# Performance work log

Measured on AMD Instinct MI355X. Metric: run time of the kernel, lower is better.

Reference implementation:

```python
import jax, jax.numpy as jnp
import numpy as np

N_WIN = 8      # windows per side (j = i = n_win)
NUM_HEADS = 8
TOPK = 4


def setup_inputs() -> dict:
    key = jax.random.key(0)
    k1, k2 = jax.random.split(key)
    cv_feature = jax.random.normal(k1, (1, 128, 128, 256), dtype=jnp.float32)
    mv_feature = jax.random.normal(k2, (1, 4, 128, 128, 256), dtype=jnp.float32)
    return {"cv_feature": cv_feature, "mv_feature": mv_feature}


def reference(cv_feature, mv_feature):
    n, H, W, C = cv_feature.shape
    v = mv_feature.shape[1]
    j = i = N_WIN
    h, w = H // j, W // i
    p2, w2 = j * i, h * w
    m = NUM_HEADS
    ch = C // m
    scale = C ** (-0.5)  # module uses d_model**-0.5 for both routing and pixel attn

    # window partition: n (j h)(i w) c -> n (j i) h w c
    cv_patch = cv_feature.reshape(n, j, h, i, w, C).transpose(0, 1, 3, 2, 4, 5).reshape(n, p2, h, w, C)
    mv_patch = mv_feature.reshape(n, v, j, h, i, w, C).transpose(0, 1, 2, 4, 3, 5, 6).reshape(n, v, p2, h, w, C)

    q_pix = cv_patch.reshape(n, p2, w2, C)          # n p2 w2 c
    kv_pix = mv_patch.reshape(n, v, p2, w2, C)      # n v p2 w2 c

    # window-level pooled queries/keys (routing is detached in the original)
    q_win = jax.lax.stop_gradient(cv_patch.mean((2, 3)))            # n p2 c
    k_win = jax.lax.stop_gradient(mv_patch.mean((3, 4)))            # n v p2 c
    k_win = k_win.reshape(n, v * p2, C)

    logits = jnp.einsum('npc,nqc->npq', q_win * scale, k_win)       # n p2 (v p2)
    topk_logit, r_idx = jax.lax.top_k(logits, TOPK)                 # n p2 k
    r_weight = jax.nn.softmax(topk_logit, axis=-1)                  # computed, unused (faithful)

    # gather routed KV windows: n p2 k w2 c
    kv_flat = kv_pix.reshape(n, v * p2, w2, C)
    kv_sel = jnp.take_along_axis(kv_flat[:, None], r_idx[:, :, :, None, None], axis=2)

    # split heads
    k_sel = kv_sel.reshape(n, p2, TOPK, w2, m, ch)                  # n p2 k w2 m ch
    q = q_pix.reshape(n, p2, w2, m, ch)                             # n p2 w2 m ch

    attn = jnp.einsum('npqmc,npkwmc->npmqkw', q * scale, k_sel)
    attn = attn.reshape(n, p2, m, w2, TOPK * w2)
    attn = jax.nn.softmax(attn, axis=-1)

    v_sel = k_sel.transpose(0, 1, 4, 2, 3, 5).reshape(n, p2, m, TOPK * w2, ch)
    out = jnp.einsum('npmqt,npmtc->npmqc', attn, v_sel)             # n p2 m w2 ch

    # merge heads + window un-partition: -> n H W C
    out = out.transpose(0, 1, 3, 2, 4).reshape(n, j, i, h, w, C)
    out = out.transpose(0, 1, 3, 2, 4, 5).reshape(n, H, W, C)
    return out
```

## Files before the change

kernel.cpp:

```cpp
#include <hip/hip_runtime.h>
#include <hip/hip_bf16.h>


typedef __attribute__((ext_vector_type(4))) float f32x4;
typedef __attribute__((ext_vector_type(8))) short s16x8;
typedef __attribute__((ext_vector_type(4))) short s16x4;
typedef __attribute__((ext_vector_type(2))) unsigned u32x2;
typedef __attribute__((ext_vector_type(4))) unsigned u32x4;

#define SCALE 0.0625f
#define LOG2E 1.44269504088896340736f

__device__ inline unsigned cvt_pk_bf16(float lo, float hi) {
  unsigned r;
  asm("v_cvt_pk_bf16_f32 %0, %1, %2" : "=v"(r) : "v"(lo), "v"(hi));
  return r;
}
__device__ inline unsigned pk_bf16_rne(float lo, float hi) {
  unsigned a = __float_as_uint(lo);
  unsigned b = __float_as_uint(hi);
  a += 0x7FFFu + ((a >> 16) & 1u);
  b += 0x7FFFu + ((b >> 16) & 1u);
  return (a >> 16) | (b & 0xFFFF0000u);
}
#if __has_builtin(__builtin_amdgcn_exp2f)
#define EXP2(x) __builtin_amdgcn_exp2f(x)
#else
#define EXP2(x) exp2f(x)
#endif

__global__ __launch_bounds__(256) void k_means(const float* __restrict__ cv,
                                               const float* __restrict__ mv,
                                               float* __restrict__ qwin,
                                               float* __restrict__ kwin) {
  __shared__ float sm[4][64];
  int wi = blockIdx.x >> 2, cq = blockIdx.x & 3;
  int pq = threadIdx.x >> 6, cl = threadIdx.x & 63;
  int c = cq * 64 + cl;
  const float* base;
  float* dst;
  if (wi < 64) {
    base = cv + ((size_t)((wi >> 3) * 16) * 128 + (wi & 7) * 16) * 256;
    dst = qwin + wi * 256;
  } else {
    int r = wi - 64;
    base = mv + (size_t)(r >> 6) * (128 * 128 * 256)
         + ((size_t)(((r >> 3) & 7) * 16) * 128 + (r & 7) * 16) * 256;
    dst = kwin + r * 256;
  }
  float s = 0.f;
  for (int k = 0; k < 64; ++k) {
    int px = pq * 64 + k;
    s += base[((px >> 4) * 128 + (px & 15)) * 256 + c];
  }
  sm[pq][cl] = s;
  __syncthreads();
  if (pq == 0)
    dst[c] = (sm[0][cl] + sm[1][cl] + sm[2][cl] + sm[3][cl]) * (1.f / 256.f);
}

__global__ __launch_bounds__(256) void k_route(const float* __restrict__ qwin,
                                               const float* __restrict__ kwin,
                                               int* __restrict__ ridx) {
  __shared__ float qrow[256];
  __shared__ float sv[256];
  __shared__ float wbv[4];
  __shared__ int wbi[4];
  int p = blockIdx.x, t = threadIdx.x;
  qrow[t] = qwin[p * 256 + t] * SCALE;
  __syncthreads();
  const f32x4* kr = reinterpret_cast<const f32x4*>(kwin + t * 256);
  float dot = 0.f;
#pragma unroll 4
  for (int c4 = 0; c4 < 64; ++c4) {
    f32x4 kv = kr[c4];
    dot += qrow[c4 * 4 + 0] * kv[0] + qrow[c4 * 4 + 1] * kv[1]
         + qrow[c4 * 4 + 2] * kv[2] + qrow[c4 * 4 + 3] * kv[3];
  }
  sv[t] = dot;
  __syncthreads();
  for (int k = 0; k < 4; ++k) {
    float v = sv[t];
    int ii = t;
#pragma unroll
    for (int off = 32; off > 0; off >>= 1) {
      float ov = __shfl_down(v, off, 64);
      int oi = __shfl_down(ii, off, 64);
      if (ov > v || (ov == v && oi < ii)) { v = ov; ii = oi; }
    }
    if ((t & 63) == 0) { wbv[t >> 6] = v; wbi[t >> 6] = ii; }
    __syncthreads();
    if (t == 0) {
      float bv = wbv[0]; int bi = wbi[0];
      for (int j = 1; j < 4; ++j)
        if (wbv[j] > bv || (wbv[j] == bv && wbi[j] < bi)) { bv = wbv[j]; bi = wbi[j]; }
      ridx[p * 4 + k] = bi;
      sv[bi] = -3.0e38f;
    }
    __syncthreads();
  }
}

__global__ __launch_bounds__(256, 2) void k_attn(const float* __restrict__ cv,
                                                 const float* __restrict__ mv,
                                                 const int* __restrict__ ridx,
                                                 float* __restrict__ out) {
  __shared__ __align__(16) short kv_lds[256 * 32];

  const int tid = threadIdx.x;
  const int lane = tid & 63, wv = tid >> 6;
  const int g = lane >> 4, c16 = lane & 15;
  const int p = blockIdx.x >> 3, m = blockIdx.x & 7;
  const int py = p >> 3, px = p & 7;

  const int4 ridx4 = *reinterpret_cast<const int4*>(ridx + p * 4);

  const float qs = SCALE * LOG2E;
  s16x8 qf[4];
#pragma unroll
  for (int qt = 0; qt < 4; ++qt) {
    const float* qp = cv + ((size_t)((py * 16 + wv * 4 + qt) * 128) + px * 16 + c16) * 256
                         + m * 32 + g * 8;
    f32x4 a = *reinterpret_cast<const f32x4*>(qp);
    f32x4 b = *reinterpret_cast<const f32x4*>(qp + 4);
    union { u32x4 u; s16x8 s; } cu;
    cu.u[0] = cvt_pk_bf16(a[0] * qs, a[1] * qs);
    cu.u[1] = cvt_pk_bf16(a[2] * qs, a[3] * qs);
    cu.u[2] = cvt_pk_bf16(b[0] * qs, b[1] * qs);
    cu.u[3] = cvt_pk_bf16(b[2] * qs, b[3] * qs);
    qf[qt] = cu.s;
  }

  f32x4 accO[4][2];
  float lsum[4];
#pragma unroll
  for (int qt = 0; qt < 4; ++qt) {
    lsum[qt] = 0.f;
    accO[qt][0] = f32x4{0.f, 0.f, 0.f, 0.f};
    accO[qt][1] = f32x4{0.f, 0.f, 0.f, 0.f};
  }
  const f32x4 zf = {0.f, 0.f, 0.f, 0.f};

  for (int w = 0; w < 4; ++w) {
    if (w) __syncthreads();
    {
      int r = (&ridx4.x)[w];
      const float* srcb = mv + (size_t)(r >> 6) * (128 * 128 * 256)
                        + ((size_t)(((r >> 3) & 7) * 16) * 128 + (r & 7) * 16) * 256 + m * 32;
#pragma unroll
      for (int i = 0; i < 8; ++i) {
        int u = i * 256 + tid;
        int pxl = u >> 3, quad = u & 7;
        f32x4 d = *reinterpret_cast<const f32x4*>(
            srcb + ((pxl >> 4) * 128 + (pxl & 15)) * 256 + quad * 4);
        u32x2 pk;
        pk[0] = cvt_pk_bf16(d[0], d[1]);
        pk[1] = cvt_pk_bf16(d[2], d[3]);
        int off = (pxl >> 2) * 128 + (quad >> 2) * 64 + (pxl & 3) * 16 + (quad & 3) * 4;
        *reinterpret_cast<u32x2*>(&kv_lds[off]) = pk;
      }
    }
    __syncthreads();

    for (int s = 0; s < 8; ++s) {
      int kr0 = s * 32 + c16;
      int kr1 = kr0 + 16;
      const s16x8 kf0 = *reinterpret_cast<const s16x8*>(
          &kv_lds[(kr0 >> 2) * 128 + (g >> 1) * 64 + (kr0 & 3) * 16 + (g & 1) * 8]);
      const s16x8 kf1 = *reinterpret_cast<const s16x8*>(
          &kv_lds[(kr1 >> 2) * 128 + (g >> 1) * 64 + (kr1 & 3) * 16 + (g & 1) * 8]);
      s16x8 V0, V1;
#pragma unroll
      for (int j = 0; j < 8; ++j) {
        int a = (s * 8 + (j >> 2) * 4 + g) * 128 + (j & 3) * 16 + c16;
        V0[j] = kv_lds[a];
        V1[j] = kv_lds[a + 64];
      }
#pragma unroll
      for (int qt = 0; qt < 4; ++qt) {
        f32x4 sx = __builtin_amdgcn_mfma_f32_16x16x32_bf16(kf0, qf[qt], zf, 0, 0, 0);
        f32x4 sy = __builtin_amdgcn_mfma_f32_16x16x32_bf16(kf1, qf[qt], zf, 0, 0, 0);
        float x0 = EXP2(sx[0]), x1 = EXP2(sx[1]), x2 = EXP2(sx[2]), x3 = EXP2(sx[3]);
        float y0 = EXP2(sy[0]), y1 = EXP2(sy[1]), y2 = EXP2(sy[2]), y3 = EXP2(sy[3]);
        lsum[qt] += ((x0 + x1) + (x2 + x3)) + ((y0 + y1) + (y2 + y3));
        union { u32x4 u; s16x8 s; } pb;
        pb.u[0] = pk_bf16_rne(x0, x1);
        pb.u[1] = pk_bf16_rne(x2, x3);
        pb.u[2] = pk_bf16_rne(y0, y1);
        pb.u[3] = pk_bf16_rne(y2, y3);
        accO[qt][0] = __builtin_amdgcn_mfma_f32_16x16x32_bf16(V0, pb.s, accO[qt][0], 0, 0, 0);
        accO[qt][1] = __builtin_amdgcn_mfma_f32_16x16x32_bf16(V1, pb.s, accO[qt][1], 0, 0, 0);
      }
    }
  }

#pragma unroll
  for (int qt = 0; qt < 4; ++qt) {
    float l = lsum[qt];
    l += __shfl_xor(l, 16, 64);
    l += __shfl_xor(l, 32, 64);
    float rl = 1.f / l;
#pragma unroll
    for (int mt = 0; mt < 2; ++mt) {
      f32x4 o = accO[qt][mt];
      o[0] *= rl; o[1] *= rl; o[2] *= rl; o[3] *= rl;
      float* op = out + ((size_t)((py * 16 + wv * 4 + qt) * 128) + px * 16 + c16) * 256
                      + m * 32 + mt * 16 + g * 4;
      *reinterpret_cast<f32x4*>(op) = o;
    }
  }
}

extern "C" void kernel_launch(void* const* d_in, const int* in_sizes, int n_in,
                              void* d_out, int out_size, void* d_ws, size_t ws_size,
                              hipStream_t stream) {
  const float* cv = (const float*)d_in[0];
  const float* mv = (const float*)d_in[1];
  float* out = (float*)d_out;

  float* qwin = (float*)d_ws;
  float* kwin = qwin + 64 * 256;
  int* ridx = (int*)(kwin + 256 * 256);

  k_means<<<1280, 256, 0, stream>>>(cv, mv, qwin, kwin);
  k_route<<<64, 256, 0, stream>>>(qwin, kwin, ridx);
  k_attn<<<512, 256, 0, stream>>>(cv, mv, ridx, out);
}
```

Before: 71.77 us.

## Vectorize window means, compute softmax denominator via MFMA, cheaper bf16 packing

The window-mean kernel now has each thread load float4 and handle half the channels per block, so it launches half as many blocks and issues fewer, wider loads. In the attention kernel the row-sum of exponentials moves from VALU adds plus cross-lane shuffles to an extra MFMA against a ones matrix. The same row sum is then available in every output lane. Probability packing to bf16 switches from round-to-nearest-even to a round-half-away add plus a byte permute, which takes fewer instructions. The trade-offs are one extra MFMA per tile and a slightly different rounding mode for the probabilities.

```diff
diff --git a/kernel.cpp b/kernel.cpp
--- a/kernel.cpp
+++ b/kernel.cpp
@@ -4,7 +4,6 @@
 
 typedef __attribute__((ext_vector_type(4))) float f32x4;
 typedef __attribute__((ext_vector_type(8))) short s16x8;
-typedef __attribute__((ext_vector_type(4))) short s16x4;
 typedef __attribute__((ext_vector_type(2))) unsigned u32x2;
 typedef __attribute__((ext_vector_type(4))) unsigned u32x4;
 
@@ -16,12 +15,10 @@
   asm("v_cvt_pk_bf16_f32 %0, %1, %2" : "=v"(r) : "v"(lo), "v"(hi));
   return r;
 }
-__device__ inline unsigned pk_bf16_rne(float lo, float hi) {
-  unsigned a = __float_as_uint(lo);
-  unsigned b = __float_as_uint(hi);
-  a += 0x7FFFu + ((a >> 16) & 1u);
-  b += 0x7FFFu + ((b >> 16) & 1u);
-  return (a >> 16) | (b & 0xFFFF0000u);
+__device__ inline unsigned pk_bf16_rna(float lo, float hi) {
+  unsigned a = __float_as_uint(lo) + 0x8000u;
+  unsigned b = __float_as_uint(hi) + 0x8000u;
+  return __builtin_amdgcn_perm(b, a, 0x07060302u);
 }
 #if __has_builtin(__builtin_amdgcn_exp2f)
 #define EXP2(x) __builtin_amdgcn_exp2f(x)
@@ -33,10 +30,9 @@
                                                const float* __restrict__ mv,
                                                float* __restrict__ qwin,
                                                float* __restrict__ kwin) {
-  __shared__ float sm[4][64];
-  int wi = blockIdx.x >> 2, cq = blockIdx.x & 3;
-  int pq = threadIdx.x >> 6, cl = threadIdx.x & 63;
-  int c = cq * 64 + cl;
+  __shared__ f32x4 sm[8][32];
+  int wi = blockIdx.x >> 1, half = blockIdx.x & 1;
+  int c4 = threadIdx.x & 31, pq = threadIdx.x >> 5;
   const float* base;
   float* dst;
   if (wi < 64) {
@@ -48,15 +44,23 @@
          + ((size_t)(((r >> 3) & 7) * 16) * 128 + (r & 7) * 16) * 256;
     dst = kwin + r * 256;
   }
-  float s = 0.f;
-  for (int k = 0; k < 64; ++k) {
-    int px = pq * 64 + k;
-    s += base[((px >> 4) * 128 + (px & 15)) * 256 + c];
-  }
-  sm[pq][cl] = s;
+  base += half * 128 + c4 * 4;
+  f32x4 acc = {0.f, 0.f, 0.f, 0.f};
+#pragma unroll 4
+  for (int k = 0; k < 32; ++k) {
+    int px = pq * 32 + k;
+    f32x4 d = *reinterpret_cast<const f32x4*>(base + ((px >> 4) * 128 + (px & 15)) * 256);
+    acc += d;
+  }
+  sm[pq][c4] = acc;
   __syncthreads();
-  if (pq == 0)
-    dst[c] = (sm[0][cl] + sm[1][cl] + sm[2][cl] + sm[3][cl]) * (1.f / 256.f);
+  if (pq == 0) {
+    f32x4 s = sm[0][c4];
+#pragma unroll
+    for (int j = 1; j < 8; ++j) s += sm[j][c4];
+    s *= (1.f / 256.f);
+    *reinterpret_cast<f32x4*>(dst + half * 128 + c4 * 4) = s;
+  }
 }
 
 __global__ __launch_bounds__(256) void k_route(const float* __restrict__ qwin,
@@ -131,11 +135,15 @@
     qf[qt] = cu.s;
   }
 
+  union { u32x4 u; s16x8 s; } ones;
+#pragma unroll
+  for (int j = 0; j < 4; ++j) ones.u[j] = 0x3F803F80u;
+
   f32x4 accO[4][2];
-  float lsum[4];
+  f32x4 accL[4];
 #pragma unroll
   for (int qt = 0; qt < 4; ++qt) {
-    lsum[qt] = 0.f;
+    accL[qt] = f32x4{0.f, 0.f, 0.f, 0.f};
     accO[qt][0] = f32x4{0.f, 0.f, 0.f, 0.f};
     accO[qt][1] = f32x4{0.f, 0.f, 0.f, 0.f};
   }
@@ -182,24 +190,21 @@
         f32x4 sy = __builtin_amdgcn_mfma_f32_16x16x32_bf16(kf1, qf[qt], zf, 0, 0, 0);
         float x0 = EXP2(sx[0]), x1 = EXP2(sx[1]), x2 = EXP2(sx[2]), x3 = EXP2(sx[3]);
         float y0 = EXP2(sy[0]), y1 = EXP2(sy[1]), y2 = EXP2(sy[2]), y3 = EXP2(sy[3]);
-        lsum[qt] += ((x0 + x1) + (x2 + x3)) + ((y0 + y1) + (y2 + y3));
         union { u32x4 u; s16x8 s; } pb;
-        pb.u[0] = pk_bf16_rne(x0, x1);
-        pb.u[1] = pk_bf16_rne(x2, x3);
-        pb.u[2] = pk_bf16_rne(y0, y1);
-        pb.u[3] = pk_bf16_rne(y2, y3);
+        pb.u[0] = pk_bf16_rna(x0, x1);
+        pb.u[1] = pk_bf16_rna(x2, x3);
+        pb.u[2] = pk_bf16_rna(y0, y1);
+        pb.u[3] = pk_bf16_rna(y2, y3);
         accO[qt][0] = __builtin_amdgcn_mfma_f32_16x16x32_bf16(V0, pb.s, accO[qt][0], 0, 0, 0);
         accO[qt][1] = __builtin_amdgcn_mfma_f32_16x16x32_bf16(V1, pb.s, accO[qt][1], 0, 0, 0);
+        accL[qt] = __builtin_amdgcn_mfma_f32_16x16x32_bf16(ones.s, pb.s, accL[qt], 0, 0, 0);
       }
     }
   }
 
 #pragma unroll
   for (int qt = 0; qt < 4; ++qt) {
-    float l = lsum[qt];
-    l += __shfl_xor(l, 16, 64);
-    l += __shfl_xor(l, 32, 64);
-    float rl = 1.f / l;
+    float rl = 1.f / accL[qt][0];
 #pragma unroll
     for (int mt = 0; mt < 2; ++mt) {
       f32x4 o = accO[qt][mt];
@@ -222,7 +227,7 @@
   float* kwin = qwin + 64 * 256;
   int* ridx = (int*)(kwin + 256 * 256);
 
-  k_means<<<1280, 256, 0, stream>>>(cv, mv, qwin, kwin);
+  k_means<<<640, 256, 0, stream>>>(cv, mv, qwin, kwin);
   k_route<<<64, 256, 0, stream>>>(qwin, kwin, ridx);
   k_attn<<<512, 256, 0, stream>>>(cv, mv, ridx, out);
 }
```

New measurement: 87.64 us. 22.1% more time.
